# Kernel optimization log

Measured on AMD Instinct MI355X. Metric: run time of the kernel, lower is better.

The kernel has to match this reference:

```python
import jax, jax.numpy as jnp
import numpy as np

B, V, SX, SY, TIN = 4, 3, 256, 256, 10
WIDTH, M1, M2, STEP, VOUT, NL = 32, 16, 16, 10, 3, 6


def setup_inputs() -> dict:
    key = jax.random.key(0)
    ks = jax.random.split(key, 20)
    n = lambda k, s, sc=1.0: sc * jax.random.normal(k, s, dtype=jnp.float32)
    u = lambda k, s: jax.random.uniform(k, s, dtype=jnp.float32)
    sc = 1.0 / WIDTH
    cshape = (NL, WIDTH, WIDTH, V, M1, M2)
    return {
        'x': n(ks[0], (B, V, SX, SY, TIN)),
        'fc0_w': n(ks[1], (TIN + 2, WIDTH), 0.1), 'fc0_b': jnp.zeros((WIDTH,), jnp.float32),
        'w1r': sc * u(ks[2], cshape), 'w1i': sc * u(ks[3], cshape),
        'w2r': sc * u(ks[4], cshape), 'w2i': sc * u(ks[5], cshape),
        'm1w': n(ks[6], (NL, WIDTH, WIDTH), 0.05), 'm1b': jnp.zeros((NL, WIDTH), jnp.float32),
        'm2w': n(ks[7], (NL, WIDTH, WIDTH), 0.05), 'm2b': jnp.zeros((NL, WIDTH), jnp.float32),
        'ww': n(ks[8], (NL, WIDTH, WIDTH), 0.05), 'wb': jnp.zeros((NL, WIDTH), jnp.float32),
        'bw': n(ks[9], (NL, WIDTH, 2), 0.1), 'bb': jnp.zeros((NL, WIDTH), jnp.float32),
        'fc1v_w': n(ks[10], (V, VOUT), 0.3), 'fc1v_b': jnp.zeros((VOUT,), jnp.float32),
        'fc1t_w': n(ks[11], (WIDTH, 256), 0.05), 'fc1t_b': jnp.zeros((256,), jnp.float32),
        'fc2t_w': n(ks[12], (256, STEP), 0.05), 'fc2t_b': jnp.zeros((STEP,), jnp.float32),
    }


def _gelu(t):
    return jax.nn.gelu(t, approximate=False)  # torch F.gelu default = exact erf


def _conv1x1(x, w, b):
    # 1x1x1 Conv3d: channel mix only. x: (b,c,v,x,y), w: (out,in)
    return jnp.einsum('bcvxy,oc->bovxy', x, w) + b[None, :, None, None, None]


def _spectral(x, w1, w2):
    # x: (b,c,v,X,Y); rfft2 over (X,Y); mode-truncated complex mix, zero-pad, irfft2
    sx, sy = x.shape[-2], x.shape[-1]
    xf = jnp.fft.rfft2(x)  # (b,c,v,X,Y//2+1) complex64
    o1 = jnp.einsum('bivxy,iovxy->bovxy', xf[..., :M1, :M2], w1)
    o2 = jnp.einsum('bivxy,iovxy->bovxy', xf[..., -M1:, :M2], w2)
    out = jnp.zeros((x.shape[0], w1.shape[1]) + xf.shape[2:], jnp.complex64)
    out = out.at[..., :M1, :M2].set(o1).at[..., -M1:, :M2].set(o2)
    return jnp.fft.irfft2(out, s=(sx, sy))


def reference(x, fc0_w, fc0_b, w1r, w1i, w2r, w2i, m1w, m1b, m2w, m2b, ww, wb, bw, bb,
              fc1v_w, fc1v_b, fc1t_w, fc1t_b, fc2t_w, fc2t_b):
    b, v, sx, sy, _ = x.shape
    gx = jnp.broadcast_to(jnp.linspace(0.0, 1.0, sx, dtype=jnp.float32)[:, None], (sx, sy))
    gy = jnp.broadcast_to(jnp.linspace(0.0, 1.0, sy, dtype=jnp.float32)[None, :], (sx, sy))
    grid = jnp.broadcast_to(jnp.stack([gx, gy], -1)[None, None], (b, v, sx, sy, 2))
    h = jnp.concatenate([x, grid], -1) @ fc0_w + fc0_b  # (b,v,X,Y,C)
    h = h.transpose(0, 4, 1, 2, 3)  # (b,C,v,X,Y)
    g = grid.transpose(0, 4, 1, 2, 3)  # (b,2,v,X,Y)

    def layer(i, t):
        x1 = _spectral(t, w1r[i] + 1j * w1i[i], w2r[i] + 1j * w2i[i])
        x1 = _conv1x1(_gelu(_conv1x1(x1, m1w[i], m1b[i])), m2w[i], m2b[i])
        x2 = _conv1x1(t, ww[i], wb[i])
        x3 = _conv1x1(g, bw[i], bb[i])
        return _gelu(x1 + x2 + x3)

    h0 = layer(0, h)
    h = layer(1, h0)
    h = layer(2, h) + h0
    h1 = layer(3, h)
    h = layer(4, h1)
    h = layer(5, h) + h1

    h = h.transpose(0, 1, 3, 4, 2)  # (b,C,X,Y,v)
    h = _gelu(h @ fc1v_w + fc1v_b)
    h = h.transpose(0, 4, 2, 3, 1)  # (b,vout,X,Y,C)
    h = _gelu(h @ fc1t_w + fc1t_b)
    return h @ fc2t_w + fc2t_b  # (b,vout,X,Y,step)
```

## Files before the change

kernel.cpp:

```cpp
#include <hip/hip_runtime.h>
#include <math.h>


#define OFF_A   0
#define OFF_B   25165824
#define OFF_T   50331648
#define OFF_XF  53477376
#define OFF_T1  54263808
#define OFF_T2T 54272000
#define OFF_TAC 54288384
#define OFF_TAS 54296576
#define OFF_TB  54304768
#define OFF_FW  54312960
#define FWSZ    4718592
#define WS_NEED_FOLD ((size_t)(OFF_FW + 4*FWSZ) * 4)

__device__ __forceinline__ float geluf(float x) {
    float a = fabsf(x) * 0.70710678118654752f;
    float t = __builtin_amdgcn_rcpf(fmaf(0.3275911f, a, 1.0f));
    float p = t * fmaf(t, fmaf(t, fmaf(t, fmaf(t, 1.061405429f, -1.453152027f),
                                       1.421413741f), -0.284496736f), 0.254829592f);
    float e = __expf(-a * a);
    float erfa = fmaf(-p, e, 1.0f);
    float er = copysignf(erfa, x);
    return 0.5f * x * (1.0f + er);
}

__global__ void k_init_tables(float* __restrict__ ws) {
    const float W0 = 6.2831853071795864769f / 256.0f;
    int stride = gridDim.x * blockDim.x;
    int tid = blockIdx.x * blockDim.x + threadIdx.x;
    for (int i = tid; i < 4096; i += stride) {
        int m = i >> 5, q = i & 31, g = q >> 2, j = q & 3;
        int k0 = 4 * (g & 3) + (g >> 2);
        int k = k0 + 2 * (j >> 1);
        float th = W0 * (float)((k * m) & 255);
        ws[OFF_T1 + i] = (j & 1) ? -sinf(th) : cosf(th);
    }
    for (int idx = tid; idx < 8192; idx += stride) {
        int n = idx >> 5, kx = idx & 31;
        int KX = (kx < 16) ? kx : (kx + 224);
        float th = W0 * (float)((KX * n) & 255);
        ws[OFF_T2T + 2*idx]     = cosf(th);
        ws[OFF_T2T + 2*idx + 1] = sinf(th);
    }
    for (int idx = tid; idx < 8192; idx += stride) {
        int kx = idx >> 8, n = idx & 255;
        int KX = (kx < 16) ? kx : (kx + 224);
        float th = W0 * (float)((KX * n) & 255);
        ws[OFF_TAC + idx] = cosf(th);
        ws[OFF_TAS + idx] = sinf(th);
    }
    for (int idx = tid; idx < 8192; idx += stride) {
        int j = idx >> 8, m = idx & 255, k = j >> 1;
        float th = W0 * (float)((k * m) & 255);
        float beta = (k == 0) ? (1.0f/65536.0f) : (2.0f/65536.0f);
        float val;
        if (j & 1) val = (k == 0) ? 0.0f : -beta * sinf(th);
        else       val = beta * cosf(th);
        ws[OFF_TB + idx] = val;
    }
}

__global__ __launch_bounds__(256) void k_foldw(const float* __restrict__ w1r,
                                               const float* __restrict__ w1i,
                                               const float* __restrict__ w2r,
                                               const float* __restrict__ w2i,
                                               const float* __restrict__ m1w,
                                               float* __restrict__ f1r, float* __restrict__ f1i,
                                               float* __restrict__ f2r, float* __restrict__ f2i) {
    int blk = blockIdx.x;
    int p = threadIdx.x;
    int op = blk & 31; int li = blk >> 5;
    int l = li >> 5;
    const float* mrow = m1w + l*1024 + op*32;
#pragma unroll
    for (int v = 0; v < 3; ++v) {
        float a1r = 0.f, a1i = 0.f, a2r = 0.f, a2i = 0.f;
#pragma unroll 4
        for (int o = 0; o < 32; ++o) {
            float mw = mrow[o];
            size_t idx = ((size_t)(li*32 + o)*3 + v)*256 + p;
            a1r = fmaf(mw, w1r[idx], a1r); a1i = fmaf(mw, w1i[idx], a1i);
            a2r = fmaf(mw, w2r[idx], a2r); a2i = fmaf(mw, w2i[idx], a2i);
        }
        size_t oidx = ((size_t)(li*32 + op)*3 + v)*256 + p;
        f1r[oidx] = a1r; f1i[oidx] = a1i; f2r[oidx] = a2r; f2i[oidx] = a2i;
    }
}

__device__ __forceinline__ void fold_lds(float* lds, int tid) {
#pragma unroll
    for (int it = 0; it < 16; ++it) {
        int pi = it * 256 + tid;
        int r = pi >> 7, mm = pi & 127;
        float* row = lds + r * 257;
        float a = row[mm], c = row[mm + 128];
        row[mm] = a + c; row[mm + 128] = a - c;
    }
}

__device__ __forceinline__ void dft_row_phase(const float* lds, const float* __restrict__ tabF,
                                              float* __restrict__ T, int b, int v, int n, int tid) {
    int r = tid >> 3, g = tid & 7;
    int p = g >> 2, idx = g & 3;
    const float* dp = lds + r * 257 + p * 128;
    const float* tp = tabF + g * 4;
    float a0 = 0.f, a1 = 0.f, a2 = 0.f, a3 = 0.f;
#pragma unroll 4
    for (int m = 0; m < 128; ++m) {
        float d = dp[m];
        float4 t = *(const float4*)(tp + m * 32);
        a0 += d * t.x; a1 += d * t.y; a2 += d * t.z; a3 += d * t.w;
    }
    size_t trow = ((size_t)((b * 32 + r) * 3 + v) * 256 + n) * 32;
    float2 w0; w0.x = a0; w0.y = a1;
    float2 w1; w1.x = a2; w1.y = a3;
    *(float2*)(T + trow + 8 * idx + 2 * p) = w0;
    *(float2*)(T + trow + 8 * idx + 2 * p + 4) = w1;
}

__global__ __launch_bounds__(256) void k_fc0(const float* __restrict__ x,
                                             const float* __restrict__ w,
                                             const float* __restrict__ bias,
                                             float* __restrict__ outA,
                                             float* __restrict__ T,
                                             const float* __restrict__ tabF) {
    __shared__ float lds[32 * 257];
    int blk = blockIdx.x;
    int m = threadIdx.x;
    int n = blk & 255;
    int bv = blk >> 8;
    int v = bv % 3, b = bv / 3;
    const float* xp = x + ((size_t)blk * 256 + m) * 10;
    float xin[10];
#pragma unroll
    for (int t = 0; t < 10; t++) xin[t] = xp[t];
    float gx = (float)n * (1.0f/255.0f), gy = (float)m * (1.0f/255.0f);
    float* op = outA + ((size_t)(b*96) + v) * 65536 + n * 256 + m;
#pragma unroll
    for (int c = 0; c < 32; c++) {
        float a = bias[c] + gx * w[10*32 + c] + gy * w[11*32 + c];
#pragma unroll
        for (int t = 0; t < 10; t++) a += xin[t] * w[t*32 + c];
        op[(size_t)c * 196608] = a;
        lds[c * 257 + m] = a;
    }
    __syncthreads();
    fold_lds(lds, m);
    __syncthreads();
    dft_row_phase(lds, tabF, T, b, v, n, m);
}

__global__ __launch_bounds__(256) void k_dft_x(const float* __restrict__ T,
                                               float* __restrict__ XFp,
                                               const float* __restrict__ tab2) {
    __shared__ float lds[4096];
    int idx = blockIdx.x;
    int half = idx & 1; int blk = idx >> 1;
    int i = blk & 31; int bv = blk >> 5;
    int b = bv / 3, v = bv - 3*b;
    int tid = threadIdx.x;
    const float4* slab = (const float4*)(T + (size_t)((b*32 + i)*3 + v) * 8192 + half * 4096);
#pragma unroll
    for (int j = 0; j < 4; ++j)
        ((float4*)lds)[j * 256 + tid] = slab[j * 256 + tid];
    __syncthreads();
    int ky = tid & 15, kxh = tid >> 4;
    const float* t2b = tab2 + half * 128 * 64;
    float r0=0.f, i0=0.f, r1=0.f, i1=0.f;
#pragma unroll 2
    for (int nn = 0; nn < 128; nn++) {
        float2 t = *(const float2*)(lds + nn * 32 + 2 * ky);
        float2 cs0 = *(const float2*)(t2b + nn*64 + kxh*2);
        float2 cs1 = *(const float2*)(t2b + nn*64 + (kxh+16)*2);
        r0 += t.x*cs0.x + t.y*cs0.y;  i0 += t.y*cs0.x - t.x*cs0.y;
        r1 += t.x*cs1.x + t.y*cs1.y;  i1 += t.y*cs1.x - t.x*cs1.y;
    }
    float2* xfp = (float2*)(XFp + (size_t)(half * 384 + blk) * 1024);
    float2 v0; v0.x = r0; v0.y = i0;
    float2 v1; v1.x = r1; v1.y = i1;
    xfp[kxh*16 + ky] = v0;
    xfp[(kxh+16)*16 + ky] = v1;
}

__global__ __launch_bounds__(256) void k_mixidft(const float* __restrict__ XFp,
                                                 float* __restrict__ T2,
                                                 const float* __restrict__ w1r,
                                                 const float* __restrict__ w1i,
                                                 const float* __restrict__ w2r,
                                                 const float* __restrict__ w2i,
                                                 const float* __restrict__ tac,
                                                 const float* __restrict__ tas, int l) {
    __shared__ float Olds[2048];
    int idx = blockIdx.x;
    int half = idx & 1; int blk = idx >> 1;
    int o = blk & 31; int bv = blk >> 5;
    int b = bv / 3, v = bv - 3*b;
    int tid = threadIdx.x;
    {
        int ky = tid & 15, kxh = tid >> 4;
        float R0=0.f, I0=0.f, R1=0.f, I1=0.f;
#pragma unroll
        for (int i = 0; i < 32; i++) {
            const float2* xa = (const float2*)(XFp + (size_t)(bv*32 + i) * 1024);
            const float2* xb = (const float2*)(XFp + (size_t)(384 + bv*32 + i) * 1024);
            float2 p0 = xa[kxh*16 + ky], q0 = xb[kxh*16 + ky];
            float2 p1 = xa[(kxh+16)*16 + ky], q1 = xb[(kxh+16)*16 + ky];
            float2 xf0; xf0.x = p0.x + q0.x; xf0.y = p0.y + q0.y;
            float2 xf1; xf1.x = p1.x + q1.x; xf1.y = p1.y + q1.y;
            size_t wbase = ((size_t)((l*32 + i)*32 + o)*3 + v) * 256;
            float a1r = w1r[wbase + tid], a1i = w1i[wbase + tid];
            float a2r = w2r[wbase + tid], a2i = w2i[wbase + tid];
            R0 += xf0.x*a1r - xf0.y*a1i;  I0 += xf0.x*a1i + xf0.y*a1r;
            R1 += xf1.x*a2r - xf1.y*a2i;  I1 += xf1.x*a2i + xf1.y*a2r;
        }
        float2 v0; v0.x = R0; v0.y = I0;
        float2 v1; v1.x = R1; v1.y = I1;
        ((float2*)Olds)[kxh*16 + ky] = v0;
        ((float2*)Olds)[(kxh+16)*16 + ky] = v1;
    }
    __syncthreads();
    {
        int ky2 = tid & 31, n8 = tid >> 5;
        int ky = ky2 >> 1, ri = ky2 & 1;
        float* t2p = T2 + (size_t)((b*32 + o)*3 + v) * 8192;
#pragma unroll 2
        for (int ii = 0; ii < 16; ++ii) {
            int n = half * 128 + ii*8 + n8;
            float acc = 0.f;
#pragma unroll
            for (int kx = 0; kx < 32; ++kx) {
                float2 ov = ((const float2*)Olds)[kx*16 + ky];
                float c = tac[kx*256 + n], s = tas[kx*256 + n];
                float ca = ri ? s : c;
                float cb = ri ? c : -s;
                acc += ov.x*ca + ov.y*cb;
            }
            t2p[n*32 + ky2] = acc;
        }
    }
}

template<int HAS_SKIP, int DO_DFT, int FOLDED>
__global__ __launch_bounds__(256) void k_conv(
    const float* IN, float* OUT, const float* SK,
    const float* __restrict__ T2, const float* __restrict__ tabB,
    const float* __restrict__ m1w, const float* __restrict__ m1b,
    const float* __restrict__ m2w, const float* __restrict__ m2b,
    const float* __restrict__ ww,  const float* __restrict__ wb,
    const float* __restrict__ bw,  const float* __restrict__ bb,
    float* __restrict__ Tout, const float* __restrict__ tabF, int l)
{
    __shared__ float lds[DO_DFT ? 32 * 257 : 1];
    int blk = blockIdx.x;
    int m = threadIdx.x;
    int n = blk & 255; int bv = blk >> 8;
    int b = bv / 3, v = bv - 3*b;

    float tb[32];
#pragma unroll
    for (int j = 0; j < 32; j++) tb[j] = tabB[j*256 + m];
    const float* t2p = T2 + (size_t)(b*96 + v) * 8192 + n * 32;
    const float* m1bl = m1b + l*32;
    float g1[32];
    if (FOLDED) {
#pragma unroll
        for (int o = 0; o < 32; o++) {
            const float* tp = t2p + o * 24576;
            float a = m1bl[o];
#pragma unroll
            for (int j = 0; j < 32; j++) a = fmaf(tp[j], tb[j], a);
            g1[o] = geluf(a);
        }
    } else {
        float x1[32];
#pragma unroll
        for (int c = 0; c < 32; c++) {
            const float* tp = t2p + c * 24576;
            float a = 0.f;
#pragma unroll
            for (int j = 0; j < 32; j++) a = fmaf(tp[j], tb[j], a);
            x1[c] = a;
        }
        const float* m1wl = m1w + l*1024;
#pragma unroll
        for (int o = 0; o < 32; o++) {
            float a = m1bl[o];
#pragma unroll
            for (int c = 0; c < 32; c++) a = fmaf(m1wl[o*32 + c], x1[c], a);
            g1[o] = geluf(a);
        }
    }

    const float* inp = IN + (size_t)(b*96 + v) * 65536 + n * 256 + m;
    float hv[32];
#pragma unroll
    for (int c = 0; c < 32; c++) hv[c] = inp[(size_t)c * 196608];

    const float* m2wl = m2w + l*1024; const float* m2bl = m2b + l*32;
    const float* wwl  = ww  + l*1024; const float* wbl  = wb  + l*32;
    const float* bwl  = bw  + l*64;   const float* bbl  = bb  + l*32;
    float gx = (float)n * (1.0f/255.0f), gy = (float)m * (1.0f/255.0f);
    float* outp = OUT + (size_t)(b*96 + v) * 65536 + n * 256 + m;
    const float* skp = SK + (size_t)(b*96 + v) * 65536 + n * 256 + m;

#pragma unroll
    for (int o = 0; o < 32; o++) {
        float a = m2bl[o] + wbl[o] + bbl[o] + bwl[o*2]*gx + bwl[o*2+1]*gy;
#pragma unroll
        for (int c = 0; c < 32; c++) a = fmaf(m2wl[o*32 + c], g1[c], a);
#pragma unroll
        for (int c = 0; c < 32; c++) a = fmaf(wwl[o*32 + c], hv[c], a);
        float val = geluf(a);
        if (HAS_SKIP) val += skp[(size_t)o * 196608];
        outp[(size_t)o * 196608] = val;
        if (DO_DFT) lds[o * 257 + m] = val;
    }
    if (DO_DFT) {
        __syncthreads();
        fold_lds(lds, m);
        __syncthreads();
        dft_row_phase(lds, tabF, Tout, b, v, n, m);
    }
}

__global__ __launch_bounds__(256) void k_final(
    const float* __restrict__ IN, float* __restrict__ OUT,
    const float* __restrict__ w1v, const float* __restrict__ b1v,
    const float* __restrict__ w1t, const float* __restrict__ b1t,
    const float* __restrict__ w2t, const float* __restrict__ b2t)
{
    int blk = blockIdx.x;
    int m = threadIdx.x;
    int vo = blk % 3; int rest = blk / 3;
    int n = rest & 255, b = rest >> 8;
    const float* inp = IN + (size_t)(b*96) * 65536 + n * 256 + m;

    float wv0 = w1v[vo], wv1 = w1v[3 + vo], wv2 = w1v[6 + vo], bv0 = b1v[vo];
    float Av[32];
#pragma unroll
    for (int c = 0; c < 32; c++) {
        float f0 = inp[(size_t)(c*3 + 0) * 65536];
        float f1 = inp[(size_t)(c*3 + 1) * 65536];
        float f2 = inp[(size_t)(c*3 + 2) * 65536];
        Av[c] = geluf(f0*wv0 + f1*wv1 + f2*wv2 + bv0);
    }

    float acc[10];
#pragma unroll
    for (int s = 0; s < 10; s++) acc[s] = 0.f;

#pragma unroll 4
    for (int u = 0; u < 256; u++) {
        float t = b1t[u];
#pragma unroll
        for (int c = 0; c < 32; c++) t = fmaf(Av[c], w1t[c*256 + u], t);
        t = geluf(t);
#pragma unroll
        for (int s = 0; s < 10; s++) acc[s] = fmaf(t, w2t[u*10 + s], acc[s]);
    }

    float* outp = OUT + ((size_t)(b*3 + vo) * 65536 + (size_t)(n * 256 + m)) * 10;
#pragma unroll
    for (int s = 0; s < 10; s++) outp[s] = acc[s] + b2t[s];
}

extern "C" void kernel_launch(void* const* d_in, const int* in_sizes, int n_in,
                              void* d_out, int out_size, void* d_ws, size_t ws_size,
                              hipStream_t stream) {
    const float* x    = (const float*)d_in[0];
    const float* fc0w = (const float*)d_in[1];
    const float* fc0b = (const float*)d_in[2];
    const float* w1r  = (const float*)d_in[3];
    const float* w1i  = (const float*)d_in[4];
    const float* w2r  = (const float*)d_in[5];
    const float* w2i  = (const float*)d_in[6];
    const float* m1w  = (const float*)d_in[7];
    const float* m1b  = (const float*)d_in[8];
    const float* m2w  = (const float*)d_in[9];
    const float* m2b  = (const float*)d_in[10];
    const float* ww   = (const float*)d_in[11];
    const float* wb   = (const float*)d_in[12];
    const float* bw   = (const float*)d_in[13];
    const float* bb   = (const float*)d_in[14];
    const float* w1v  = (const float*)d_in[15];
    const float* b1v  = (const float*)d_in[16];
    const float* w1t  = (const float*)d_in[17];
    const float* b1t  = (const float*)d_in[18];
    const float* w2t  = (const float*)d_in[19];
    const float* b2t  = (const float*)d_in[20];

    float* ws   = (float*)d_ws;
    float* A    = ws + OFF_A;
    float* Bu   = ws + OFF_B;
    float* T    = ws + OFF_T;
    float* XFp  = ws + OFF_XF;
    float* tabF = ws + OFF_T1;
    float* tab2 = ws + OFF_T2T;
    float* tac  = ws + OFF_TAC;
    float* tas  = ws + OFF_TAS;
    float* tbB  = ws + OFF_TB;

    const bool fold = ws_size >= WS_NEED_FOLD;
    float* f1r = ws + OFF_FW;
    float* f1i = ws + OFF_FW + FWSZ;
    float* f2r = ws + OFF_FW + 2*FWSZ;
    float* f2i = ws + OFF_FW + 3*FWSZ;

    k_init_tables<<<64, 256, 0, stream>>>(ws);
    if (fold)
        k_foldw<<<6144, 256, 0, stream>>>(w1r, w1i, w2r, w2i, m1w, f1r, f1i, f2r, f2i);
    k_fc0<<<3072, 256, 0, stream>>>(x, fc0w, fc0b, A, T, tabF);

    const float* u1r = fold ? f1r : w1r;  const float* u1i = fold ? f1i : w1i;
    const float* u2r = fold ? f2r : w2r;  const float* u2i = fold ? f2i : w2i;

    float* lin [6] = {A, A, Bu, Bu, A, Bu};
    float* lout[6] = {A, Bu, Bu, A, Bu, Bu};
    const float* lskip[6] = {nullptr, nullptr, A, nullptr, nullptr, A};

    for (int l = 0; l < 6; l++) {
        k_dft_x<<<768, 256, 0, stream>>>(T, XFp, tab2);
        k_mixidft<<<768, 256, 0, stream>>>(XFp, T, u1r, u1i, u2r, u2i, tac, tas, l);
        int skip = lskip[l] != nullptr, dodft = (l < 5);
        if (fold) {
            if (skip && dodft)
                k_conv<1,1,1><<<3072, 256, 0, stream>>>(lin[l], lout[l], lskip[l], T, tbB,
                                                        m1w, m1b, m2w, m2b, ww, wb, bw, bb, T, tabF, l);
            else if (!skip && dodft)
                k_conv<0,1,1><<<3072, 256, 0, stream>>>(lin[l], lout[l], nullptr, T, tbB,
                                                        m1w, m1b, m2w, m2b, ww, wb, bw, bb, T, tabF, l);
            else if (skip && !dodft)
                k_conv<1,0,1><<<3072, 256, 0, stream>>>(lin[l], lout[l], lskip[l], T, tbB,
                                                        m1w, m1b, m2w, m2b, ww, wb, bw, bb, T, tabF, l);
            else
                k_conv<0,0,1><<<3072, 256, 0, stream>>>(lin[l], lout[l], nullptr, T, tbB,
                                                        m1w, m1b, m2w, m2b, ww, wb, bw, bb, T, tabF, l);
        } else {
            if (skip && dodft)
                k_conv<1,1,0><<<3072, 256, 0, stream>>>(lin[l], lout[l], lskip[l], T, tbB,
                                                        m1w, m1b, m2w, m2b, ww, wb, bw, bb, T, tabF, l);
            else if (!skip && dodft)
                k_conv<0,1,0><<<3072, 256, 0, stream>>>(lin[l], lout[l], nullptr, T, tbB,
                                                        m1w, m1b, m2w, m2b, ww, wb, bw, bb, T, tabF, l);
            else if (skip && !dodft)
                k_conv<1,0,0><<<3072, 256, 0, stream>>>(lin[l], lout[l], lskip[l], T, tbB,
                                                        m1w, m1b, m2w, m2b, ww, wb, bw, bb, T, tabF, l);
            else
                k_conv<0,0,0><<<3072, 256, 0, stream>>>(lin[l], lout[l], nullptr, T, tbB,
                                                        m1w, m1b, m2w, m2b, ww, wb, bw, bb, T, tabF, l);
        }
    }

    k_final<<<3072, 256, 0, stream>>>(Bu, (float*)d_out, w1v, b1v, w1t, b1t, w2t, b2t);
}
```

Before: 2.464 ms.

## Relayout spectral intermediate into output buffer and vectorize weight/table loads

Stores the inverse-DFT intermediate in a new row-contiguous layout in the output buffer, so each conv thread reads its 32x32 spectral block with contiguous float4 loads instead of strided scalar loads. Interleaves the cos/sin tables and the folded complex weights as float2 pairs, and pre-transposes fc1t weights so the final kernel can read them as float4. In k_conv the channel loads for the conv are moved ahead of the GELU stage and the channel-mix loops are vectorized. This reuses the output buffer as scratch, which relies on the final kernel overwriting it, and the wider per-thread accumulator arrays may raise register pressure.

Result: slower. 2.582 ms (+4.8%).

```diff
diff --git a/kernel.cpp b/kernel.cpp
--- a/kernel.cpp
+++ b/kernel.cpp
@@ -8,11 +8,12 @@
 #define OFF_XF  53477376
 #define OFF_T1  54263808
 #define OFF_T2T 54272000
-#define OFF_TAC 54288384
-#define OFF_TAS 54296576
+#define OFF_TCS 54288384
 #define OFF_TB  54304768
-#define OFF_FW  54312960
+#define OFF_WT  54312960
+#define OFF_FW  54321152
 #define FWSZ    4718592
+#define WS_NEED_WT   ((size_t)OFF_FW * 4)
 #define WS_NEED_FOLD ((size_t)(OFF_FW + 4*FWSZ) * 4)
 
 __device__ __forceinline__ float geluf(float x) {
@@ -26,7 +27,7 @@
     return 0.5f * x * (1.0f + er);
 }
 
-__global__ void k_init_tables(float* __restrict__ ws) {
+__global__ void k_init_tables(float* __restrict__ ws, const float* __restrict__ w1t, int do_wt) {
     const float W0 = 6.2831853071795864769f / 256.0f;
     int stride = gridDim.x * blockDim.x;
     int tid = blockIdx.x * blockDim.x + threadIdx.x;
@@ -48,8 +49,8 @@
         int kx = idx >> 8, n = idx & 255;
         int KX = (kx < 16) ? kx : (kx + 224);
         float th = W0 * (float)((KX * n) & 255);
-        ws[OFF_TAC + idx] = cosf(th);
-        ws[OFF_TAS + idx] = sinf(th);
+        ws[OFF_TCS + 2*idx]     = cosf(th);
+        ws[OFF_TCS + 2*idx + 1] = sinf(th);
     }
     for (int idx = tid; idx < 8192; idx += stride) {
         int j = idx >> 8, m = idx & 255, k = j >> 1;
@@ -60,6 +61,10 @@
         else       val = beta * cosf(th);
         ws[OFF_TB + idx] = val;
     }
+    if (do_wt) {
+        for (int idx = tid; idx < 8192; idx += stride)
+            ws[OFF_WT + idx] = w1t[(idx & 31) * 256 + (idx >> 5)];
+    }
 }
 
 __global__ __launch_bounds__(256) void k_foldw(const float* __restrict__ w1r,
@@ -67,8 +72,8 @@
                                                const float* __restrict__ w2r,
                                                const float* __restrict__ w2i,
                                                const float* __restrict__ m1w,
-                                               float* __restrict__ f1r, float* __restrict__ f1i,
-                                               float* __restrict__ f2r, float* __restrict__ f2i) {
+                                               float2* __restrict__ fp1,
+                                               float2* __restrict__ fp2) {
     int blk = blockIdx.x;
     int p = threadIdx.x;
     int op = blk & 31; int li = blk >> 5;
@@ -85,7 +90,9 @@
             a2r = fmaf(mw, w2r[idx], a2r); a2i = fmaf(mw, w2i[idx], a2i);
         }
         size_t oidx = ((size_t)(li*32 + op)*3 + v)*256 + p;
-        f1r[oidx] = a1r; f1i[oidx] = a1i; f2r[oidx] = a2r; f2i[oidx] = a2i;
+        float2 u1; u1.x = a1r; u1.y = a1i;
+        float2 u2; u2.x = a2r; u2.y = a2i;
+        fp1[oidx] = u1; fp2[oidx] = u2;
     }
 }
 
@@ -184,14 +191,16 @@
     xfp[(kxh+16)*16 + ky] = v1;
 }
 
+template<int FOLDW>
 __global__ __launch_bounds__(256) void k_mixidft(const float* __restrict__ XFp,
-                                                 float* __restrict__ T2,
+                                                 float* __restrict__ T2B,
                                                  const float* __restrict__ w1r,
                                                  const float* __restrict__ w1i,
                                                  const float* __restrict__ w2r,
                                                  const float* __restrict__ w2i,
-                                                 const float* __restrict__ tac,
-                                                 const float* __restrict__ tas, int l) {
+                                                 const float2* __restrict__ fp1,
+                                                 const float2* __restrict__ fp2,
+                                                 const float2* __restrict__ tcs, int l) {
     __shared__ float Olds[2048];
     int idx = blockIdx.x;
     int half = idx & 1; int blk = idx >> 1;
@@ -210,8 +219,14 @@
             float2 xf0; xf0.x = p0.x + q0.x; xf0.y = p0.y + q0.y;
             float2 xf1; xf1.x = p1.x + q1.x; xf1.y = p1.y + q1.y;
             size_t wbase = ((size_t)((l*32 + i)*32 + o)*3 + v) * 256;
-            float a1r = w1r[wbase + tid], a1i = w1i[wbase + tid];
-            float a2r = w2r[wbase + tid], a2i = w2i[wbase + tid];
+            float a1r, a1i, a2r, a2i;
+            if (FOLDW) {
+                float2 u1 = fp1[wbase + tid]; float2 u2 = fp2[wbase + tid];
+                a1r = u1.x; a1i = u1.y; a2r = u2.x; a2i = u2.y;
+            } else {
+                a1r = w1r[wbase + tid]; a1i = w1i[wbase + tid];
+                a2r = w2r[wbase + tid]; a2i = w2i[wbase + tid];
+            }
             R0 += xf0.x*a1r - xf0.y*a1i;  I0 += xf0.x*a1i + xf0.y*a1r;
             R1 += xf1.x*a2r - xf1.y*a2i;  I1 += xf1.x*a2i + xf1.y*a2r;
         }
@@ -224,7 +239,7 @@
     {
         int ky2 = tid & 31, n8 = tid >> 5;
         int ky = ky2 >> 1, ri = ky2 & 1;
-        float* t2p = T2 + (size_t)((b*32 + o)*3 + v) * 8192;
+        float* base = T2B + (size_t)(b*3 + v) * 262144 + o*32;
 #pragma unroll 2
         for (int ii = 0; ii < 16; ++ii) {
             int n = half * 128 + ii*8 + n8;
@@ -232,12 +247,12 @@
 #pragma unroll
             for (int kx = 0; kx < 32; ++kx) {
                 float2 ov = ((const float2*)Olds)[kx*16 + ky];
-                float c = tac[kx*256 + n], s = tas[kx*256 + n];
-                float ca = ri ? s : c;
-                float cb = ri ? c : -s;
+                float2 cs = tcs[kx*256 + n];
+                float ca = ri ? cs.y : cs.x;
+                float cb = ri ? cs.x : -cs.y;
                 acc += ov.x*ca + ov.y*cb;
             }
-            t2p[n*32 + ky2] = acc;
+            base[(size_t)n*1024 + ky2] = acc;
         }
     }
 }
@@ -245,7 +260,7 @@
 template<int HAS_SKIP, int DO_DFT, int FOLDED>
 __global__ __launch_bounds__(256) void k_conv(
     const float* IN, float* OUT, const float* SK,
-    const float* __restrict__ T2, const float* __restrict__ tabB,
+    const float* __restrict__ T2B, const float* __restrict__ tabB,
     const float* __restrict__ m1w, const float* __restrict__ m1b,
     const float* __restrict__ m2w, const float* __restrict__ m2b,
     const float* __restrict__ ww,  const float* __restrict__ wb,
@@ -261,42 +276,50 @@
     float tb[32];
 #pragma unroll
     for (int j = 0; j < 32; j++) tb[j] = tabB[j*256 + m];
-    const float* t2p = T2 + (size_t)(b*96 + v) * 8192 + n * 32;
+    const float* t2row = T2B + (size_t)(bv) * 262144 + (size_t)n * 1024;
     const float* m1bl = m1b + l*32;
+    float acc[32];
+#pragma unroll
+    for (int o = 0; o < 32; o++) {
+        const float4* q = (const float4*)(t2row + o*32);
+        float a = 0.f;
+#pragma unroll
+        for (int jj = 0; jj < 8; jj++) {
+            float4 qv = q[jj];
+            a = fmaf(qv.x, tb[jj*4+0], a);
+            a = fmaf(qv.y, tb[jj*4+1], a);
+            a = fmaf(qv.z, tb[jj*4+2], a);
+            a = fmaf(qv.w, tb[jj*4+3], a);
+        }
+        acc[o] = a;
+    }
+
+    const float* inp = IN + (size_t)(b*96 + v) * 65536 + n * 256 + m;
+    float hv[32];
+#pragma unroll
+    for (int c = 0; c < 32; c++) hv[c] = inp[(size_t)c * 196608];
+
     float g1[32];
     if (FOLDED) {
 #pragma unroll
+        for (int o = 0; o < 32; o++) g1[o] = geluf(acc[o] + m1bl[o]);
+    } else {
+        const float* m1wl = m1w + l*1024;
+#pragma unroll
         for (int o = 0; o < 32; o++) {
-            const float* tp = t2p + o * 24576;
+            const float4* mq = (const float4*)(m1wl + o*32);
             float a = m1bl[o];
 #pragma unroll
-            for (int j = 0; j < 32; j++) a = fmaf(tp[j], tb[j], a);
+            for (int c4 = 0; c4 < 8; c4++) {
+                float4 wv = mq[c4];
+                a = fmaf(wv.x, acc[c4*4+0], a);
+                a = fmaf(wv.y, acc[c4*4+1], a);
+                a = fmaf(wv.z, acc[c4*4+2], a);
+                a = fmaf(wv.w, acc[c4*4+3], a);
+            }
             g1[o] = geluf(a);
         }
-    } else {
-        float x1[32];
-#pragma unroll
-        for (int c = 0; c < 32; c++) {
-            const float* tp = t2p + c * 24576;
-            float a = 0.f;
-#pragma unroll
-            for (int j = 0; j < 32; j++) a = fmaf(tp[j], tb[j], a);
-            x1[c] = a;
-        }
-        const float* m1wl = m1w + l*1024;
-#pragma unroll
-        for (int o = 0; o < 32; o++) {
-            float a = m1bl[o];
-#pragma unroll
-            for (int c = 0; c < 32; c++) a = fmaf(m1wl[o*32 + c], x1[c], a);
-            g1[o] = geluf(a);
-        }
-    }
-
-    const float* inp = IN + (size_t)(b*96 + v) * 65536 + n * 256 + m;
-    float hv[32];
-#pragma unroll
-    for (int c = 0; c < 32; c++) hv[c] = inp[(size_t)c * 196608];
+    }
 
     const float* m2wl = m2w + l*1024; const float* m2bl = m2b + l*32;
     const float* wwl  = ww  + l*1024; const float* wbl  = wb  + l*32;
@@ -307,11 +330,25 @@
 
 #pragma unroll
     for (int o = 0; o < 32; o++) {
+        const float4* mq = (const float4*)(m2wl + o*32);
+        const float4* wq = (const float4*)(wwl + o*32);
         float a = m2bl[o] + wbl[o] + bbl[o] + bwl[o*2]*gx + bwl[o*2+1]*gy;
 #pragma unroll
-        for (int c = 0; c < 32; c++) a = fmaf(m2wl[o*32 + c], g1[c], a);
-#pragma unroll
-        for (int c = 0; c < 32; c++) a = fmaf(wwl[o*32 + c], hv[c], a);
+        for (int c4 = 0; c4 < 8; c4++) {
+            float4 wv = mq[c4];
+            a = fmaf(wv.x, g1[c4*4+0], a);
+            a = fmaf(wv.y, g1[c4*4+1], a);
+            a = fmaf(wv.z, g1[c4*4+2], a);
+            a = fmaf(wv.w, g1[c4*4+3], a);
+        }
+#pragma unroll
+        for (int c4 = 0; c4 < 8; c4++) {
+            float4 wv = wq[c4];
+            a = fmaf(wv.x, hv[c4*4+0], a);
+            a = fmaf(wv.y, hv[c4*4+1], a);
+            a = fmaf(wv.z, hv[c4*4+2], a);
+            a = fmaf(wv.w, hv[c4*4+3], a);
+        }
         float val = geluf(a);
         if (HAS_SKIP) val += skp[(size_t)o * 196608];
         outp[(size_t)o * 196608] = val;
@@ -325,6 +362,7 @@
     }
 }
 
+template<int TR>
 __global__ __launch_bounds__(256) void k_final(
     const float* __restrict__ IN, float* __restrict__ OUT,
     const float* __restrict__ w1v, const float* __restrict__ b1v,
@@ -354,8 +392,20 @@
 #pragma unroll 4
     for (int u = 0; u < 256; u++) {
         float t = b1t[u];
-#pragma unroll
-        for (int c = 0; c < 32; c++) t = fmaf(Av[c], w1t[c*256 + u], t);
+        if (TR) {
+            const float4* wr = (const float4*)(w1t + u*32);
+#pragma unroll
+            for (int c4 = 0; c4 < 8; c4++) {
+                float4 wv = wr[c4];
+                t = fmaf(Av[c4*4+0], wv.x, t);
+                t = fmaf(Av[c4*4+1], wv.y, t);
+                t = fmaf(Av[c4*4+2], wv.z, t);
+                t = fmaf(Av[c4*4+3], wv.w, t);
+            }
+        } else {
+#pragma unroll
+            for (int c = 0; c < 32; c++) t = fmaf(Av[c], w1t[c*256 + u], t);
+        }
         t = geluf(t);
 #pragma unroll
         for (int s = 0; s < 10; s++) acc[s] = fmaf(t, w2t[u*10 + s], acc[s]);
@@ -398,23 +448,21 @@
     float* XFp  = ws + OFF_XF;
     float* tabF = ws + OFF_T1;
     float* tab2 = ws + OFF_T2T;
-    float* tac  = ws + OFF_TAC;
-    float* tas  = ws + OFF_TAS;
+    const float2* tcs = (const float2*)(ws + OFF_TCS);
     float* tbB  = ws + OFF_TB;
-
-    const bool fold = ws_size >= WS_NEED_FOLD;
-    float* f1r = ws + OFF_FW;
-    float* f1i = ws + OFF_FW + FWSZ;
-    float* f2r = ws + OFF_FW + 2*FWSZ;
-    float* f2i = ws + OFF_FW + 3*FWSZ;
-
-    k_init_tables<<<64, 256, 0, stream>>>(ws);
+    float* w1tT = ws + OFF_WT;
+
+    float* T2B = (float*)d_out;
+
+    const bool do_wt = ws_size >= WS_NEED_WT;
+    const bool fold  = ws_size >= WS_NEED_FOLD;
+    float2* fp1 = (float2*)(ws + OFF_FW);
+    float2* fp2 = (float2*)(ws + OFF_FW + 2*FWSZ);
+
+    k_init_tables<<<64, 256, 0, stream>>>(ws, w1t, do_wt ? 1 : 0);
     if (fold)
-        k_foldw<<<6144, 256, 0, stream>>>(w1r, w1i, w2r, w2i, m1w, f1r, f1i, f2r, f2i);
+        k_foldw<<<6144, 256, 0, stream>>>(w1r, w1i, w2r, w2i, m1w, fp1, fp2);
     k_fc0<<<3072, 256, 0, stream>>>(x, fc0w, fc0b, A, T, tabF);
-
-    const float* u1r = fold ? f1r : w1r;  const float* u1i = fold ? f1i : w1i;
-    const float* u2r = fold ? f2r : w2r;  const float* u2i = fold ? f2i : w2i;
 
     float* lin [6] = {A, A, Bu, Bu, A, Bu};
     float* lout[6] = {A, Bu, Bu, A, Bu, Bu};
@@ -422,36 +470,42 @@
 
     for (int l = 0; l < 6; l++) {
         k_dft_x<<<768, 256, 0, stream>>>(T, XFp, tab2);
-        k_mixidft<<<768, 256, 0, stream>>>(XFp, T, u1r, u1i, u2r, u2i, tac, tas, l);
+        if (fold)
+            k_mixidft<1><<<768, 256, 0, stream>>>(XFp, T2B, w1r, w1i, w2r, w2i, fp1, fp2, tcs, l);
+        else
+            k_mixidft<0><<<768, 256, 0, stream>>>(XFp, T2B, w1r, w1i, w2r, w2i, fp1, fp2, tcs, l);
         int skip = lskip[l] != nullptr, dodft = (l < 5);
         if (fold) {
             if (skip && dodft)
-                k_conv<1,1,1><<<3072, 256, 0, stream>>>(lin[l], lout[l], lskip[l], T, tbB,
+                k_conv<1,1,1><<<3072, 256, 0, stream>>>(lin[l], lout[l], lskip[l], T2B, tbB,
                                                         m1w, m1b, m2w, m2b, ww, wb, bw, bb, T, tabF, l);
             else if (!skip && dodft)
-                k_conv<0,1,1><<<3072, 256, 0, stream>>>(lin[l], lout[l], nullptr, T, tbB,
+                k_conv<0,1,1><<<3072, 256, 0, stream>>>(lin[l], lout[l], nullptr, T2B, tbB,
                                                         m1w, m1b, m2w, m2b, ww, wb, bw, bb, T, tabF, l);
             else if (skip && !dodft)
-                k_conv<1,0,1><<<3072, 256, 0, stream>>>(lin[l], lout[l], lskip[l], T, tbB,
+                k_conv<1,0,1><<<3072, 256, 0, stream>>>(lin[l], lout[l], lskip[l], T2B, tbB,
                                                         m1w, m1b, m2w, m2b, ww, wb, bw, bb, T, tabF, l);
             else
-                k_conv<0,0,1><<<3072, 256, 0, stream>>>(lin[l], lout[l], nullptr, T, tbB,
+                k_conv<0,0,1><<<3072, 256, 0, stream>>>(lin[l], lout[l], nullptr, T2B, tbB,
                                                         m1w, m1b, m2w, m2b, ww, wb, bw, bb, T, tabF, l);
         } else {
             if (skip && dodft)
-                k_conv<1,1,0><<<3072, 256, 0, stream>>>(lin[l], lout[l], lskip[l], T, tbB,
+                k_conv<1,1,0><<<3072, 256, 0, stream>>>(lin[l], lout[l], lskip[l], T2B, tbB,
                                                         m1w, m1b, m2w, m2b, ww, wb, bw, bb, T, tabF, l);
             else if (!skip && dodft)
-                k_conv<0,1,0><<<3072, 256, 0, stream>>>(lin[l], lout[l], nullptr, T, tbB,
+                k_conv<0,1,0><<<3072, 256, 0, stream>>>(lin[l], lout[l], nullptr, T2B, tbB,
                                                         m1w, m1b, m2w, m2b, ww, wb, bw, bb, T, tabF, l);
             else if (skip && !dodft)
-                k_conv<1,0,0><<<3072, 256, 0, stream>>>(lin[l], lout[l], lskip[l], T, tbB,
+                k_conv<1,0,0><<<3072, 256, 0, stream>>>(lin[l], lout[l], lskip[l], T2B, tbB,
                                                         m1w, m1b, m2w, m2b, ww, wb, bw, bb, T, tabF, l);
             else
-                k_conv<0,0,0><<<3072, 256, 0, stream>>>(lin[l], lout[l], nullptr, T, tbB,
-                                                        m1w, m1b, m2w, m2b, ww, wb, bw, bb, T, tabF, l);
-        }
-    }
-
-    k_final<<<3072, 256, 0, stream>>>(Bu, (float*)d_out, w1v, b1v, w1t, b1t, w2t, b2t);
-}
+                k_conv<0,0,0><<<3072, 256, 0, stream>>>(lin[l], lout[l], nullptr, T2B, tbB,
+                                                        m1w, m1b, m2w, m2b, ww, wb, bw, bb, T, tabF, l);
+        }
+    }
+
+    if (do_wt)
+        k_final<1><<<3072, 256, 0, stream>>>(Bu, (float*)d_out, w1v, b1v, w1tT, b1t, w2t, b2t);
+    else
+        k_final<0><<<3072, 256, 0, stream>>>(Bu, (float*)d_out, w1v, b1v, w1t, b1t, w2t, b2t);
+}
```
